# Kernel tuning notes

Hardware: AMD Instinct MI355X
Metric: run time of the kernel (lower is better)

Reference implementation:

```python
import jax, jax.numpy as jnp
import numpy as np
from jax import lax

NUM_HEADS = 8
FOCUSING_FACTOR = 3.0
KERNEL_SIZE = 5


def setup_inputs() -> dict:
    key = jax.random.key(0)
    ks = jax.random.split(key, 9)
    B, C, H, W = 16, 256, 64, 64
    s = 0.02
    return {
        "x": jax.random.normal(ks[0], (B, C, H, W), dtype=jnp.float32),
        "Wq": jax.random.normal(ks[1], (C, C), dtype=jnp.float32) * s,
        "bq": jax.random.normal(ks[2], (C,), dtype=jnp.float32) * s,
        "Wkv": jax.random.normal(ks[3], (2 * C, C), dtype=jnp.float32) * s,
        "bkv": jax.random.normal(ks[4], (2 * C,), dtype=jnp.float32) * s,
        "Wproj": jax.random.normal(ks[5], (C, C), dtype=jnp.float32) * s,
        "bproj": jax.random.normal(ks[6], (C,), dtype=jnp.float32) * s,
        "dwc_w": jax.random.normal(ks[7], (C // NUM_HEADS, 1, KERNEL_SIZE, KERNEL_SIZE), dtype=jnp.float32) * s,
        "dwc_b": jax.random.normal(ks[8], (C // NUM_HEADS,), dtype=jnp.float32) * s,
        "scale_param": jnp.zeros((1, 1, C), dtype=jnp.float32),
    }


def reference(x, Wq, bq, Wkv, bkv, Wproj, bproj, dwc_w, dwc_b, scale_param):
    B, C, H, W = x.shape
    nh = NUM_HEADS
    hd = C // nh
    N = H * W
    num = int(round(N ** 0.5))  # feature map side, N is a perfect square

    xt = x.reshape(B, C, N).transpose(0, 2, 1)  # [B, N, C]
    q = xt @ Wq.T + bq
    kv = xt @ Wkv.T + bkv  # [B, N, 2C] -> (2, C) split on last dim
    k, v = kv[..., :C], kv[..., C:]
    # positional_encoding is freshly-initialized zeros in the original forward -> no-op

    scale = jax.nn.softplus(scale_param)  # [1, 1, C]
    q = (jax.nn.relu(q) + 1e-6) / scale
    k = (jax.nn.relu(k) + 1e-6) / scale
    q_norm = jnp.linalg.norm(q, axis=-1, keepdims=True)
    k_norm = jnp.linalg.norm(k, axis=-1, keepdims=True)
    q = q ** FOCUSING_FACTOR
    k = k ** FOCUSING_FACTOR
    q = q / jnp.linalg.norm(q, axis=-1, keepdims=True) * q_norm
    k = k / jnp.linalg.norm(k, axis=-1, keepdims=True) * k_norm

    def split_heads(t):  # [B, N, C] -> [B*nh, N, hd]
        return t.reshape(B, N, nh, hd).transpose(0, 2, 1, 3).reshape(B * nh, N, hd)

    q, k, v = split_heads(q), split_heads(k), split_heads(v)

    # linear attention (kv path; i*j*(c+d) > c*d*(i+j) for these shapes)
    z = 1.0 / (jnp.einsum('bic,bc->bi', q, k.sum(axis=1)) + 1e-6)  # [BH, N]
    kv_state = jnp.einsum('bjc,bjd->bcd', k, v)  # [BH, hd, hd]
    out = jnp.einsum('bic,bcd->bid', q, kv_state) * z[..., None]  # [BH, N, hd]

    # depthwise conv on v feature map
    fm = v.transpose(0, 2, 1).reshape(B * nh, hd, num, num)
    fm = lax.conv_general_dilated(
        fm, dwc_w, window_strides=(1, 1),
        padding=[(KERNEL_SIZE // 2, KERNEL_SIZE // 2)] * 2,
        dimension_numbers=('NCHW', 'OIHW', 'NCHW'),
        feature_group_count=hd,
    ) + dwc_b[None, :, None, None]
    fm = fm.reshape(B * nh, hd, N).transpose(0, 2, 1)  # [BH, N, hd]

    out = out + fm
    out = out.reshape(B, nh, N, hd).transpose(0, 2, 1, 3).reshape(B, N, C)
    out = out @ Wproj.T + bproj
    return out.transpose(0, 2, 1).reshape(B, C, H, W)
```

## Files before the change

### kernel.cpp

```cpp
#include <hip/hip_runtime.h>
#include <math.h>

#define NB 16
#define NC 256
#define NN 4096
#define HD 32
#define BHD 128
#define KSPLIT 4

typedef unsigned short bf16_t;
typedef __attribute__((ext_vector_type(4))) float floatx4;
typedef __attribute__((ext_vector_type(8))) short shortx8;

__device__ __forceinline__ float bf2f(unsigned int u16) {
  return __uint_as_float(u16 << 16);
}
__device__ __forceinline__ bf16_t f2bf(float f) {
  unsigned int u = __float_as_uint(f);
  return (bf16_t)((u + 0x7FFFu + ((u >> 16) & 1u)) >> 16);
}
__device__ __forceinline__ void bf8_expand(uint4 u, float* f) {
  f[0] = bf2f(u.x & 0xffffu); f[1] = bf2f(u.x >> 16);
  f[2] = bf2f(u.y & 0xffffu); f[3] = bf2f(u.y >> 16);
  f[4] = bf2f(u.z & 0xffffu); f[5] = bf2f(u.z >> 16);
  f[6] = bf2f(u.w & 0xffffu); f[7] = bf2f(u.w >> 16);
}
__device__ __forceinline__ float softplusf(float x) {
  return fmaxf(x, 0.0f) + log1pf(expf(-fabsf(x)));
}

__device__ __forceinline__ void gl_lds16(const void* g, void* l) {
  __builtin_amdgcn_global_load_lds(
      (const __attribute__((address_space(1))) unsigned int*)g,
      (__attribute__((address_space(3))) unsigned int*)l, 16, 0, 0);
}

__global__ __launch_bounds__(256) void k_prepx(
    const float* __restrict__ x, bf16_t* __restrict__ xbf)
{
  __shared__ float T[64][68];
  const int tid = threadIdx.x;
  const int n0 = blockIdx.x * 64, c0 = blockIdx.y * 64, b = blockIdx.z;
  const float* xb = x + (size_t)b * NC * NN;
#pragma unroll
  for (int it = 0; it < 4; ++it) {
    int c = it * 16 + (tid >> 4);
    int n4 = (tid & 15) * 4;
    float4 v = *(const float4*)(xb + (size_t)(c0 + c) * NN + n0 + n4);
    T[c][n4 + 0] = v.x; T[c][n4 + 1] = v.y;
    T[c][n4 + 2] = v.z; T[c][n4 + 3] = v.w;
  }
  __syncthreads();
  bf16_t* ob = xbf + (size_t)b * NN * NC;
#pragma unroll
  for (int it = 0; it < 2; ++it) {
    int n = it * 32 + (tid >> 3);
    int ch = (tid & 7) * 8;
    unsigned short e[8];
#pragma unroll
    for (int j = 0; j < 8; ++j) e[j] = f2bf(T[ch + j][n]);
    uint4 u;
    u.x = e[0] | ((unsigned)e[1] << 16); u.y = e[2] | ((unsigned)e[3] << 16);
    u.z = e[4] | ((unsigned)e[5] << 16); u.w = e[6] | ((unsigned)e[7] << 16);
    *(uint4*)(ob + (size_t)(n0 + n) * NC + c0 + ch) = u;
  }
}

__global__ __launch_bounds__(256) void k_prepw(
    const float* __restrict__ Wq, const float* __restrict__ Wkv,
    const float* __restrict__ Wp, const float* __restrict__ bq,
    const float* __restrict__ bkv, const float* __restrict__ sp,
    bf16_t* __restrict__ Wqkvb, bf16_t* __restrict__ Wpb,
    float* __restrict__ bias768, float* __restrict__ rscale)
{
  const int blk = blockIdx.x;
  const int tid = threadIdx.x;
  if (blk < 768) {
    const float* src = (blk < 256) ? (Wq + (size_t)blk * NC)
                                   : (Wkv + (size_t)(blk - 256) * NC);
    Wqkvb[(size_t)blk * NC + tid] = f2bf(src[tid]);
  } else if (blk < 1024) {
    int j = blk - 768;
    Wpb[(size_t)j * NC + tid] = f2bf(Wp[(size_t)j * NC + tid]);
  } else if (blk == 1024) {
    for (int i = tid; i < 768; i += 256)
      bias768[i] = (i < 256) ? bq[i] : bkv[i - 256];
  } else {
    rscale[tid] = 1.0f / softplusf(sp[tid]);
  }
}

__global__ __launch_bounds__(256) void k_qkv_mfma(
    const bf16_t* __restrict__ xbf, const bf16_t* __restrict__ Wqkvb,
    const float* __restrict__ bias768, bf16_t* __restrict__ qkv)
{
  __shared__ bf16_t As[128 * 32];
  __shared__ bf16_t Bs[128 * 32];
  const int tid = threadIdx.x;
  const int lane = tid & 63;
  const int w = tid >> 6;
  const int b = blockIdx.z;
  const int m0 = blockIdx.x * 128;
  const int n0 = blockIdx.y * 128;
  const bf16_t* Ab = xbf + ((size_t)b * NN + m0) * NC;
  const bf16_t* Bb = Wqkvb + (size_t)n0 * NC;

  const int wm = (w & 1) * 64;
  const int wn = (w >> 1) * 64;
  const int srow = w * 32 + (lane >> 2);
  const int scol = (lane & 3) * 8;
  const int fm = lane & 15;
  const int kg = lane >> 4;

  floatx4 acc[4][4];
#pragma unroll
  for (int i = 0; i < 4; ++i)
#pragma unroll
    for (int j = 0; j < 4; ++j) {
      floatx4 z = {0.f, 0.f, 0.f, 0.f};
      acc[i][j] = z;
    }

  for (int k0 = 0; k0 < NC; k0 += 32) {
#pragma unroll
    for (int r = 0; r < 2; ++r) {
      gl_lds16(Ab + (size_t)(srow + r * 16) * NC + k0 + scol,
               &As[(w * 32 + r * 16) * 32]);
      gl_lds16(Bb + (size_t)(srow + r * 16) * NC + k0 + scol,
               &Bs[(w * 32 + r * 16) * 32]);
    }
    __syncthreads();
    shortx8 af[4], bfg[4];
#pragma unroll
    for (int t = 0; t < 4; ++t) {
      af[t]  = *(const shortx8*)&As[(wm + t * 16 + fm) * 32 + kg * 8];
      bfg[t] = *(const shortx8*)&Bs[(wn + t * 16 + fm) * 32 + kg * 8];
    }
#pragma unroll
    for (int tm = 0; tm < 4; ++tm)
#pragma unroll
      for (int tn = 0; tn < 4; ++tn)
        acc[tm][tn] = __builtin_amdgcn_mfma_f32_16x16x32_bf16(
            af[tm], bfg[tn], acc[tm][tn], 0, 0, 0);
    __syncthreads();
  }

  float bv[4];
#pragma unroll
  for (int tn = 0; tn < 4; ++tn)
    bv[tn] = bias768[n0 + wn + tn * 16 + fm];

  bf16_t* obase = qkv + ((size_t)b * NN + m0) * 768;
#pragma unroll
  for (int tm = 0; tm < 4; ++tm) {
    int mrow = wm + tm * 16 + kg * 4;
#pragma unroll
    for (int tn = 0; tn < 4; ++tn) {
      int n = n0 + wn + tn * 16 + fm;
#pragma unroll
      for (int r = 0; r < 4; ++r)
        obase[(size_t)(mrow + r) * 768 + n] = f2bf(acc[tm][tn][r] + bv[tn]);
    }
  }
}

__global__ __launch_bounds__(256) void k_focus(
    bf16_t* __restrict__ qkv, const float* __restrict__ rscale)
{
  const int lane = threadIdx.x & 63;
  const int w = threadIdx.x >> 6;
  const size_t t = (size_t)blockIdx.x * 4 + w;
  bf16_t* row = qkv + t * 768;
  ushort4 qu = *(ushort4*)(row + lane * 4);
  ushort4 ku = *(ushort4*)(row + 256 + lane * 4);
  float4 s4 = *(const float4*)(rscale + lane * 4);
  float q[4] = {bf2f(qu.x), bf2f(qu.y), bf2f(qu.z), bf2f(qu.w)};
  float k[4] = {bf2f(ku.x), bf2f(ku.y), bf2f(ku.z), bf2f(ku.w)};
  float rs[4] = {s4.x, s4.y, s4.z, s4.w};
  float q3[4], k3[4];
  float sq2 = 0.f, sq6 = 0.f, sk2 = 0.f, sk6 = 0.f;
#pragma unroll
  for (int i = 0; i < 4; ++i) {
    float qi = (fmaxf(q[i], 0.f) + 1e-6f) * rs[i];
    float ki = (fmaxf(k[i], 0.f) + 1e-6f) * rs[i];
    float qc = qi * qi * qi;
    float kc = ki * ki * ki;
    sq2 += qi * qi;  sk2 += ki * ki;
    sq6 += qc * qc;  sk6 += kc * kc;
    q3[i] = qc; k3[i] = kc;
  }
#pragma unroll
  for (int off = 32; off > 0; off >>= 1) {
    sq2 += __shfl_xor(sq2, off);
    sq6 += __shfl_xor(sq6, off);
    sk2 += __shfl_xor(sk2, off);
    sk6 += __shfl_xor(sk6, off);
  }
  float qs = sqrtf(sq2) * rsqrtf(sq6);
  float ks = sqrtf(sk2) * rsqrtf(sk6);
  ushort4 qo, ko;
  qo.x = f2bf(q3[0] * qs); qo.y = f2bf(q3[1] * qs);
  qo.z = f2bf(q3[2] * qs); qo.w = f2bf(q3[3] * qs);
  ko.x = f2bf(k3[0] * ks); ko.y = f2bf(k3[1] * ks);
  ko.z = f2bf(k3[2] * ks); ko.w = f2bf(k3[3] * ks);
  *(ushort4*)(row + lane * 4) = qo;
  *(ushort4*)(row + 256 + lane * 4) = ko;
}

__global__ __launch_bounds__(256) void k_kvstate(
    const bf16_t* __restrict__ qkv, float* __restrict__ kvsp,
    float* __restrict__ ksump)
{
  const int bh = blockIdx.x;
  const int spl = blockIdx.y;
  const int b = bh >> 3, h = bh & 7;
  __shared__ float ks[64][36];
  __shared__ float vs[64][36];
  const int tid = threadIdx.x;
  const int c = tid >> 3;
  const int d4 = (tid & 7) * 4;
  float acc0 = 0.f, acc1 = 0.f, acc2 = 0.f, acc3 = 0.f, ksacc = 0.f;
  const int t0base = spl * (NN / KSPLIT);
  for (int t0 = t0base; t0 < t0base + NN / KSPLIT; t0 += 64) {
#pragma unroll
    for (int r = 0; r < 2; ++r) {
      int idx = r * 256 + tid;
      int tok = idx >> 3;
      int slot = idx & 7;
      const bf16_t* rowp = qkv + ((size_t)b * NN + t0 + tok) * 768 + 256 + h * HD;
      uint4 u;
      float f[8];
      if (slot < 4) {
        u = *(const uint4*)(rowp + slot * 8);
        bf8_expand(u, f);
#pragma unroll
        for (int e = 0; e < 8; ++e) ks[tok][slot * 8 + e] = f[e];
      } else {
        u = *(const uint4*)(rowp + 256 + (slot - 4) * 8);
        bf8_expand(u, f);
#pragma unroll
        for (int e = 0; e < 8; ++e) vs[tok][(slot - 4) * 8 + e] = f[e];
      }
    }
    __syncthreads();
#pragma unroll 4
    for (int t = 0; t < 64; ++t) {
      float kc = ks[t][c];
      float vv[4];
      *(float4*)vv = *(const float4*)&vs[t][d4];
      acc0 += kc * vv[0]; acc1 += kc * vv[1];
      acc2 += kc * vv[2]; acc3 += kc * vv[3];
      ksacc += kc;
    }
    __syncthreads();
  }
  float o[4] = {acc0, acc1, acc2, acc3};
  *(float4*)(kvsp + ((size_t)spl * BHD + bh) * (HD * HD) + c * HD + d4) = *(float4*)o;
  if (d4 == 0) ksump[((size_t)spl * BHD + bh) * HD + c] = ksacc;
}

__global__ __launch_bounds__(256) void k_combine(
    const float* __restrict__ kvsp, const float* __restrict__ ksump,
    bf16_t* __restrict__ kvTb, bf16_t* __restrict__ ksumb)
{
  const int bh = blockIdx.x;
  const int tid = threadIdx.x;
  const int c = tid >> 3;
  const int d4 = (tid & 7) * 4;
  float v[4] = {0.f, 0.f, 0.f, 0.f};
#pragma unroll
  for (int s = 0; s < KSPLIT; ++s) {
    const float* p = kvsp + ((size_t)s * BHD + bh) * (HD * HD) + c * HD + d4;
#pragma unroll
    for (int e = 0; e < 4; ++e) v[e] += p[e];
  }
#pragma unroll
  for (int e = 0; e < 4; ++e)
    kvTb[(size_t)bh * (HD * HD) + (d4 + e) * HD + c] = f2bf(v[e]);
  if (d4 == 0) {
    float u = 0.f;
#pragma unroll
    for (int s = 0; s < KSPLIT; ++s) u += ksump[((size_t)s * BHD + bh) * HD + c];
    ksumb[(size_t)bh * HD + c] = f2bf(u);
  }
}

#define VT_STRIDE 548
__global__ __launch_bounds__(256) void k_attnout(
    const bf16_t* __restrict__ qkv, const bf16_t* __restrict__ kvTb,
    const bf16_t* __restrict__ ksumb, const float* __restrict__ dwc_w,
    const float* __restrict__ dwc_b, bf16_t* __restrict__ attn)
{
  __shared__ bf16_t vt[32 * VT_STRIDE];
  __shared__ bf16_t mvz[256 * 32];
  const int tid = threadIdx.x;
  const int lane = tid & 63;
  const int w = tid >> 6;
  const int s = blockIdx.x;
  const int bh = blockIdx.y;
  const int b = bh >> 3, h = bh & 7;

#pragma unroll
  for (int it = 0; it < 8; ++it) {
    int idx = it * 256 + tid;
    int ry = idx >> 8;
    int col = (idx >> 2) & 63;
    int slot = idx & 3;
    int y = s * 4 - 2 + ry;
    uint4 u = make_uint4(0u, 0u, 0u, 0u);
    if (y >= 0 && y < 64)
      u = *(const uint4*)(qkv + ((size_t)b * NN + y * 64 + col) * 768 + 512 + h * HD + slot * 8);
    unsigned short e[8];
    e[0] = (unsigned short)(u.x & 0xffffu); e[1] = (unsigned short)(u.x >> 16);
    e[2] = (unsigned short)(u.y & 0xffffu); e[3] = (unsigned short)(u.y >> 16);
    e[4] = (unsigned short)(u.z & 0xffffu); e[5] = (unsigned short)(u.z >> 16);
    e[6] = (unsigned short)(u.w & 0xffffu); e[7] = (unsigned short)(u.w >> 16);
#pragma unroll
    for (int j = 0; j < 8; ++j)
      vt[(slot * 8 + j) * VT_STRIDE + (col + 2) * 8 + ry] = e[j];
  }
#pragma unroll
  for (int e = 0; e < 4; ++e) {
    int idx = tid * 4 + e;
    int d = idx >> 5;
    int rem = idx & 31;
    int cc4 = rem >> 3;
    int ry = rem & 7;
    int cc = (cc4 < 2) ? cc4 : (64 + cc4);
    vt[d * VT_STRIDE + cc * 8 + ry] = 0;
  }

  const int fm = lane & 15;
  const int kg = lane >> 4;
  shortx8 b0 = *(const shortx8*)(kvTb + (size_t)bh * 1024 + fm * HD + kg * 8);
  shortx8 b1 = *(const shortx8*)(kvTb + (size_t)bh * 1024 + (16 + fm) * HD + kg * 8);
  shortx8 b2 = {0, 0, 0, 0, 0, 0, 0, 0};
  if (fm == 0) b2 = *(const shortx8*)(ksumb + (size_t)bh * HD + kg * 8);
  floatx4 zf = {0.f, 0.f, 0.f, 0.f};
#pragma unroll
  for (int q = 0; q < 4; ++q) {
    int mt = w * 4 + q;
    int tok = s * 256 + mt * 16 + fm;
    shortx8 a = *(const shortx8*)(qkv + ((size_t)b * NN + tok) * 768 + h * HD + kg * 8);
    floatx4 d0 = __builtin_amdgcn_mfma_f32_16x16x32_bf16(a, b0, zf, 0, 0, 0);
    floatx4 d1 = __builtin_amdgcn_mfma_f32_16x16x32_bf16(a, b1, zf, 0, 0, 0);
    floatx4 d2 = __builtin_amdgcn_mfma_f32_16x16x32_bf16(a, b2, zf, 0, 0, 0);
#pragma unroll
    for (int r = 0; r < 4; ++r) {
      float qk = __shfl(d2[r], lane & 48);
      float z = 1.0f / (qk + 1e-6f);
      int tl = mt * 16 + kg * 4 + r;
      mvz[tl * 32 + fm] = f2bf(d0[r] * z);
      mvz[tl * 32 + 16 + fm] = f2bf(d1[r] * z);
    }
  }
  __syncthreads();

  const int d = tid & 31;
  const int xg = tid >> 5;
  const int x0c = xg * 8;
  float wr[25];
#pragma unroll
  for (int j = 0; j < 25; ++j) wr[j] = dwc_w[d * 25 + j];
  const float bd = dwc_b[d];
  const bf16_t* vd = vt + d * VT_STRIDE;

  float win[5][8];
#define LOADCOL(dst, cc) do {                                   \
    const bf16_t* _p = vd + (cc) * 8;                           \
    uint2 _u0 = *(const uint2*)_p;                              \
    uint2 _u1 = *(const uint2*)(_p + 4);                        \
    (dst)[0] = bf2f(_u0.x & 0xffffu); (dst)[1] = bf2f(_u0.x >> 16); \
    (dst)[2] = bf2f(_u0.y & 0xffffu); (dst)[3] = bf2f(_u0.y >> 16); \
    (dst)[4] = bf2f(_u1.x & 0xffffu); (dst)[5] = bf2f(_u1.x >> 16); \
    (dst)[6] = bf2f(_u1.y & 0xffffu); (dst)[7] = bf2f(_u1.y >> 16); \
  } while (0)

#pragma unroll
  for (int p = 0; p < 4; ++p) LOADCOL(win[p], x0c + p);

  bf16_t* arow = attn + ((size_t)b * NN + s * 256) * NC + h * HD + d;
#pragma unroll
  for (int i = 0; i < 8; ++i) {
    int x = x0c + i;
    LOADCOL(win[4], x + 4);
#pragma unroll
    for (int ty = 0; ty < 4; ++ty) {
      float acc = bd;
#pragma unroll
      for (int ky = 0; ky < 5; ++ky)
#pragma unroll
        for (int kx = 0; kx < 5; ++kx)
          acc += wr[ky * 5 + kx] * win[kx][ty + ky];
      int tl = ty * 64 + x;
      acc += bf2f(mvz[tl * 32 + d]);
      arow[(size_t)tl * NC] = f2bf(acc);
    }
#pragma unroll
    for (int c2 = 0; c2 < 4; ++c2)
#pragma unroll
      for (int r2 = 0; r2 < 8; ++r2) win[c2][r2] = win[c2 + 1][r2];
  }
#undef LOADCOL
}

__global__ __launch_bounds__(256) void k_proj_mfma(
    const bf16_t* __restrict__ attn, const bf16_t* __restrict__ Wpb,
    const float* __restrict__ bp, float* __restrict__ out)
{
  __shared__ bf16_t As[128 * 32];
  __shared__ bf16_t Bs[128 * 32];
  const int tid = threadIdx.x;
  const int lane = tid & 63;
  const int w = tid >> 6;
  const size_t m0 = (size_t)blockIdx.x * 128;
  const int n0 = blockIdx.y * 128;
  const bf16_t* Ab = attn + m0 * NC;
  const bf16_t* Bb = Wpb + (size_t)n0 * NC;

  const int wm = (w & 1) * 64;
  const int wn = (w >> 1) * 64;
  const int srow = w * 32 + (lane >> 2);
  const int scol = (lane & 3) * 8;
  const int fm = lane & 15;
  const int kg = lane >> 4;

  floatx4 acc[4][4];
#pragma unroll
  for (int i = 0; i < 4; ++i)
#pragma unroll
    for (int j = 0; j < 4; ++j) {
      floatx4 z = {0.f, 0.f, 0.f, 0.f};
      acc[i][j] = z;
    }

  for (int k0 = 0; k0 < NC; k0 += 32) {
#pragma unroll
    for (int r = 0; r < 2; ++r) {
      gl_lds16(Ab + (size_t)(srow + r * 16) * NC + k0 + scol,
               &As[(w * 32 + r * 16) * 32]);
      gl_lds16(Bb + (size_t)(srow + r * 16) * NC + k0 + scol,
               &Bs[(w * 32 + r * 16) * 32]);
    }
    __syncthreads();
    shortx8 af[4], bfg[4];
#pragma unroll
    for (int t = 0; t < 4; ++t) {
      af[t]  = *(const shortx8*)&As[(wm + t * 16 + fm) * 32 + kg * 8];
      bfg[t] = *(const shortx8*)&Bs[(wn + t * 16 + fm) * 32 + kg * 8];
    }
#pragma unroll
    for (int tm = 0; tm < 4; ++tm)
#pragma unroll
      for (int tn = 0; tn < 4; ++tn)
        acc[tm][tn] = __builtin_amdgcn_mfma_f32_16x16x32_bf16(
            af[tm], bfg[tn], acc[tm][tn], 0, 0, 0);
    __syncthreads();
  }

  const int b = (int)(m0 >> 12);
  const int t0 = (int)(m0 & 4095);
  float* ob = out + (size_t)b * NC * NN;
#pragma unroll
  for (int tn = 0; tn < 4; ++tn) {
    int j = n0 + wn + tn * 16 + fm;
    float bj = bp[j];
#pragma unroll
    for (int tm = 0; tm < 4; ++tm) {
      int trow = t0 + wm + tm * 16 + kg * 4;
      float4 o;
      o.x = acc[tm][tn][0] + bj;
      o.y = acc[tm][tn][1] + bj;
      o.z = acc[tm][tn][2] + bj;
      o.w = acc[tm][tn][3] + bj;
      *(float4*)(ob + (size_t)j * NN + trow) = o;
    }
  }
}

extern "C" void kernel_launch(void* const* d_in, const int* in_sizes, int n_in,
                              void* d_out, int out_size, void* d_ws, size_t ws_size,
                              hipStream_t stream)
{
  (void)in_sizes; (void)n_in; (void)out_size; (void)ws_size;
  const float* x    = (const float*)d_in[0];
  const float* Wq   = (const float*)d_in[1];
  const float* bq   = (const float*)d_in[2];
  const float* Wkv  = (const float*)d_in[3];
  const float* bkv  = (const float*)d_in[4];
  const float* Wp   = (const float*)d_in[5];
  const float* bp   = (const float*)d_in[6];
  const float* dwcw = (const float*)d_in[7];
  const float* dwcb = (const float*)d_in[8];
  const float* sp   = (const float*)d_in[9];
  float* out = (float*)d_out;

  char* wsb = (char*)d_ws;
  bf16_t* qkv  = (bf16_t*)wsb;
  bf16_t* attn = (bf16_t*)(wsb + 100663296u);
  bf16_t* xbf  = attn;
  float*  kvsp = (float*)(wsb + 100663296u + 33554432u);
  float*  ksump = kvsp + (size_t)KSPLIT * BHD * HD * HD;
  bf16_t* kvTb  = (bf16_t*)(ksump + (size_t)KSPLIT * BHD * HD);
  bf16_t* ksumb = kvTb + (size_t)BHD * HD * HD;
  bf16_t* Wqkvb = ksumb + (size_t)BHD * HD;
  bf16_t* Wpb   = Wqkvb + 768 * 256;
  float*  bias768 = (float*)(Wpb + 256 * 256);
  float*  rscale  = bias768 + 768;

  k_prepx<<<dim3(64, 4, 16), 256, 0, stream>>>(x, xbf);
  k_prepw<<<1026, 256, 0, stream>>>(Wq, Wkv, Wp, bq, bkv, sp, Wqkvb, Wpb, bias768, rscale);
  k_qkv_mfma<<<dim3(32, 6, 16), 256, 0, stream>>>(xbf, Wqkvb, bias768, qkv);
  k_focus<<<16384, 256, 0, stream>>>(qkv, rscale);
  k_kvstate<<<dim3(BHD, KSPLIT), 256, 0, stream>>>(qkv, kvsp, ksump);
  k_combine<<<BHD, 256, 0, stream>>>(kvsp, ksump, kvTb, ksumb);
  k_attnout<<<dim3(16, BHD), 256, 0, stream>>>(qkv, kvTb, ksumb, dwcw, dwcb, attn);
  k_proj_mfma<<<dim3(512, 2), 256, 0, stream>>>(attn, Wpb, bp, out);
}
```

Measured before the change: 313.4 us.

## Compute kv-state with MFMA per wavefront and widen token split

Replaces the LDS-staged scalar FMA outer product in k_kvstate with a per-wavefront 32x32x16 bf16 MFMA that reads K and V straight from global memory, with each wave owning one token split. KSPLIT rises from 4 to 32 for more parallelism, and k_combine is reworked to one thread per output element reducing across 32 partials. Partial buffers move into the attn workspace region, which is free at that point. This trades FP32 accumulation of bf16 inputs via FMA for MFMA, and uses strided 2-byte global loads that may coalesce poorly.

```diff
diff --git a/kernel.cpp b/kernel.cpp
--- a/kernel.cpp
+++ b/kernel.cpp
@@ -6,10 +6,11 @@
 #define NN 4096
 #define HD 32
 #define BHD 128
-#define KSPLIT 4
+#define KSPLIT 32
 
 typedef unsigned short bf16_t;
 typedef __attribute__((ext_vector_type(4))) float floatx4;
+typedef __attribute__((ext_vector_type(16))) float floatx16;
 typedef __attribute__((ext_vector_type(8))) short shortx8;
 
 __device__ __forceinline__ float bf2f(unsigned int u16) {
@@ -211,77 +212,70 @@
     const bf16_t* __restrict__ qkv, float* __restrict__ kvsp,
     float* __restrict__ ksump)
 {
+  const int tid = threadIdx.x;
+  const int lane = tid & 63;
+  const int w = tid >> 6;
   const int bh = blockIdx.x;
-  const int spl = blockIdx.y;
+  const int spl = blockIdx.y * 4 + w;
   const int b = bh >> 3, h = bh & 7;
-  __shared__ float ks[64][36];
-  __shared__ float vs[64][36];
-  const int tid = threadIdx.x;
-  const int c = tid >> 3;
-  const int d4 = (tid & 7) * 4;
-  float acc0 = 0.f, acc1 = 0.f, acc2 = 0.f, acc3 = 0.f, ksacc = 0.f;
-  const int t0base = spl * (NN / KSPLIT);
-  for (int t0 = t0base; t0 < t0base + NN / KSPLIT; t0 += 64) {
-#pragma unroll
-    for (int r = 0; r < 2; ++r) {
-      int idx = r * 256 + tid;
-      int tok = idx >> 3;
-      int slot = idx & 7;
-      const bf16_t* rowp = qkv + ((size_t)b * NN + t0 + tok) * 768 + 256 + h * HD;
-      uint4 u;
-      float f[8];
-      if (slot < 4) {
-        u = *(const uint4*)(rowp + slot * 8);
-        bf8_expand(u, f);
-#pragma unroll
-        for (int e = 0; e < 8; ++e) ks[tok][slot * 8 + e] = f[e];
-      } else {
-        u = *(const uint4*)(rowp + 256 + (slot - 4) * 8);
-        bf8_expand(u, f);
-#pragma unroll
-        for (int e = 0; e < 8; ++e) vs[tok][(slot - 4) * 8 + e] = f[e];
-      }
-    }
-    __syncthreads();
-#pragma unroll 4
-    for (int t = 0; t < 64; ++t) {
-      float kc = ks[t][c];
-      float vv[4];
-      *(float4*)vv = *(const float4*)&vs[t][d4];
-      acc0 += kc * vv[0]; acc1 += kc * vv[1];
-      acc2 += kc * vv[2]; acc3 += kc * vv[3];
-      ksacc += kc;
-    }
-    __syncthreads();
-  }
-  float o[4] = {acc0, acc1, acc2, acc3};
-  *(float4*)(kvsp + ((size_t)spl * BHD + bh) * (HD * HD) + c * HD + d4) = *(float4*)o;
-  if (d4 == 0) ksump[((size_t)spl * BHD + bh) * HD + c] = ksacc;
+  const int c = lane & 31;
+  const int g = lane >> 5;
+
+  floatx16 acc;
+#pragma unroll
+  for (int r = 0; r < 16; ++r) acc[r] = 0.f;
+  float ksacc = 0.f;
+
+  const bf16_t* kp = qkv + ((size_t)b * NN + (size_t)spl * (NN / KSPLIT) + g * 8) * 768
+                     + 256 + h * HD + c;
+#pragma unroll 2
+  for (int s = 0; s < (NN / KSPLIT) / 16; ++s) {
+    unsigned short av[8], bv[8];
+#pragma unroll
+    for (int e = 0; e < 8; ++e) {
+      av[e] = kp[(size_t)e * 768];
+      bv[e] = kp[(size_t)e * 768 + 256];
+    }
+    shortx8 af, bfg;
+#pragma unroll
+    for (int e = 0; e < 8; ++e) {
+      af[e] = (short)av[e];
+      bfg[e] = (short)bv[e];
+      ksacc += bf2f(av[e]);
+    }
+    acc = __builtin_amdgcn_mfma_f32_32x32x16_bf16(af, bfg, acc, 0, 0, 0);
+    kp += 16 * 768;
+  }
+
+  float* op = kvsp + ((size_t)spl * BHD + bh) * (HD * HD);
+#pragma unroll
+  for (int r = 0; r < 16; ++r) {
+    int row = (r & 3) + 8 * (r >> 2) + 4 * g;
+    op[row * HD + c] = acc[r];
+  }
+  ksacc += __shfl_xor(ksacc, 32);
+  if (g == 0) ksump[((size_t)spl * BHD + bh) * HD + c] = ksacc;
 }
 
 __global__ __launch_bounds__(256) void k_combine(
     const float* __restrict__ kvsp, const float* __restrict__ ksump,
     bf16_t* __restrict__ kvTb, bf16_t* __restrict__ ksumb)
 {
-  const int bh = blockIdx.x;
-  const int tid = threadIdx.x;
-  const int c = tid >> 3;
-  const int d4 = (tid & 7) * 4;
-  float v[4] = {0.f, 0.f, 0.f, 0.f};
-#pragma unroll
-  for (int s = 0; s < KSPLIT; ++s) {
-    const float* p = kvsp + ((size_t)s * BHD + bh) * (HD * HD) + c * HD + d4;
-#pragma unroll
-    for (int e = 0; e < 4; ++e) v[e] += p[e];
-  }
-#pragma unroll
-  for (int e = 0; e < 4; ++e)
-    kvTb[(size_t)bh * (HD * HD) + (d4 + e) * HD + c] = f2bf(v[e]);
-  if (d4 == 0) {
+  const int gid = blockIdx.x * 256 + threadIdx.x;
+  const int bh = gid >> 10;
+  const int cd = gid & 1023;
+  const int cc = cd >> 5, d = cd & 31;
+  float v = 0.f;
+  const float* p = kvsp + (size_t)bh * (HD * HD) + cd;
+#pragma unroll
+  for (int s = 0; s < KSPLIT; ++s) v += p[(size_t)s * BHD * (HD * HD)];
+  kvTb[(size_t)bh * (HD * HD) + d * HD + cc] = f2bf(v);
+  if (cd < HD) {
     float u = 0.f;
-#pragma unroll
-    for (int s = 0; s < KSPLIT; ++s) u += ksump[((size_t)s * BHD + bh) * HD + c];
-    ksumb[(size_t)bh * HD + c] = f2bf(u);
+    const float* q = ksump + (size_t)bh * HD + cd;
+#pragma unroll
+    for (int s = 0; s < KSPLIT; ++s) u += q[(size_t)s * BHD * HD];
+    ksumb[(size_t)bh * HD + cd] = f2bf(u);
   }
 }
 
@@ -499,9 +493,10 @@
   bf16_t* qkv  = (bf16_t*)wsb;
   bf16_t* attn = (bf16_t*)(wsb + 100663296u);
   bf16_t* xbf  = attn;
-  float*  kvsp = (float*)(wsb + 100663296u + 33554432u);
-  float*  ksump = kvsp + (size_t)KSPLIT * BHD * HD * HD;
-  bf16_t* kvTb  = (bf16_t*)(ksump + (size_t)KSPLIT * BHD * HD);
+  float*  kvsp  = (float*)attn;
+  float*  ksump = (float*)(wsb + 100663296u + 16777216u);
+  char*   tail  = wsb + 100663296u + 33554432u + 2097152u + 65536u;
+  bf16_t* kvTb  = (bf16_t*)tail;
   bf16_t* ksumb = kvTb + (size_t)BHD * HD * HD;
   bf16_t* Wqkvb = ksumb + (size_t)BHD * HD;
   bf16_t* Wpb   = Wqkvb + 768 * 256;
@@ -512,8 +507,8 @@
   k_prepw<<<1026, 256, 0, stream>>>(Wq, Wkv, Wp, bq, bkv, sp, Wqkvb, Wpb, bias768, rscale);
   k_qkv_mfma<<<dim3(32, 6, 16), 256, 0, stream>>>(xbf, Wqkvb, bias768, qkv);
   k_focus<<<16384, 256, 0, stream>>>(qkv, rscale);
-  k_kvstate<<<dim3(BHD, KSPLIT), 256, 0, stream>>>(qkv, kvsp, ksump);
-  k_combine<<<BHD, 256, 0, stream>>>(kvsp, ksump, kvTb, ksumb);
+  k_kvstate<<<dim3(BHD, KSPLIT / 4), 256, 0, stream>>>(qkv, kvsp, ksump);
+  k_combine<<<512, 256, 0, stream>>>(kvsp, ksump, kvTb, ksumb);
   k_attnout<<<dim3(16, BHD), 256, 0, stream>>>(qkv, kvTb, ksumb, dwcw, dwcb, attn);
   k_proj_mfma<<<dim3(512, 2), 256, 0, stream>>>(attn, Wpb, bp, out);
 }
```

After: 288.7 us. 7.9% less time.
